# Kernel optimization log

Hardware: AMD Instinct MI355X
Metric: run time of the kernel (lower is better)

Reference implementation:

```python
import jax, jax.numpy as jnp
import numpy as np

N_NODES = 100000
N_EDGES = 1600000
IN_FEATS = 64
HIDDEN = 32
OUT_FEATS = 40


def _linear_init(key, fan_in, fan_out):
    kw, kb = jax.random.split(key)
    bound = 1.0 / np.sqrt(fan_in)
    W = jax.random.uniform(kw, (fan_in, fan_out), jnp.float32, -bound, bound)
    b = jax.random.uniform(kb, (fan_out,), jnp.float32, -bound, bound)
    return W, b


def setup_inputs() -> dict:
    key = jax.random.key(0)
    ks = jax.random.split(key, 8)
    x = jax.random.normal(ks[0], (N_NODES, IN_FEATS), jnp.float32)
    edge_index = jax.random.randint(ks[1], (2, N_EDGES), 0, N_NODES, jnp.int64)
    W_self1, b_self1 = _linear_init(ks[2], IN_FEATS, HIDDEN)
    W_neigh1, b_neigh1 = _linear_init(ks[3], IN_FEATS, HIDDEN)
    W_self2, b_self2 = _linear_init(ks[4], HIDDEN, HIDDEN)
    W_neigh2, b_neigh2 = _linear_init(ks[5], HIDDEN, HIDDEN)
    W_out, b_out = _linear_init(ks[6], HIDDEN, OUT_FEATS)
    W_lin1, b_lin1 = _linear_init(ks[7], IN_FEATS, OUT_FEATS)
    return {"x": x, "edge_index": edge_index,
            "W_self1": W_self1, "b_self1": b_self1,
            "W_neigh1": W_neigh1, "b_neigh1": b_neigh1,
            "W_self2": W_self2, "b_self2": b_self2,
            "W_neigh2": W_neigh2, "b_neigh2": b_neigh2,
            "W_out": W_out, "b_out": b_out,
            "W_lin1": W_lin1, "b_lin1": b_lin1}


def _scatter_mean(feats, src, dst, num_nodes):
    # gather neighbor features [E, F], sum into destinations, divide by degree
    msgs = feats[src]
    agg = jax.ops.segment_sum(msgs, dst, num_segments=num_nodes)
    cnt = jax.ops.segment_sum(jnp.ones((src.shape[0],), feats.dtype), dst,
                              num_segments=num_nodes)
    return agg / jnp.maximum(cnt, 1.0)[:, None]


def _intra_conv(h, src, dst, W_self, b_self, W_neigh, b_neigh, num_nodes):
    # scatter-mean aggregation + fused linear/residual(self)/relu
    x_self = h @ W_self + b_self
    neigh = _scatter_mean(h, src, dst, num_nodes)
    out = neigh @ W_neigh + b_neigh + x_self
    return jax.nn.relu(out)


def reference(x, edge_index, W_self1, b_self1, W_neigh1, b_neigh1,
              W_self2, b_self2, W_neigh2, b_neigh2, W_out, b_out,
              W_lin1, b_lin1):
    num_nodes = x.shape[0]
    src, dst = edge_index[0], edge_index[1]  # PyG source_to_target flow
    initial_x = x @ W_lin1 + b_lin1  # computed in original forward (unused in output)
    h = _intra_conv(x, src, dst, W_self1, b_self1, W_neigh1, b_neigh1, num_nodes)
    h = _intra_conv(h, src, dst, W_self2, b_self2, W_neigh2, b_neigh2, num_nodes)
    # hidden dim == 32 so x32 is the last layer's output (== h); dropout is eval no-op
    x32 = h
    logits = h @ W_out + b_out
    return (x32, logits)
```

## Files before the change

### kernel.cpp

```cpp
#include <hip/hip_runtime.h>

#define NN 100000
#define NE 1600000
#define RB 256
#define NPB 391
#define CAP 8192
#define GS 32

typedef unsigned int uint;
typedef unsigned short ushort;
typedef __fp16 fp16x2 __attribute__((ext_vector_type(2)));

__device__ __forceinline__ float blo(uint u){ return __uint_as_float(u << 16); }
__device__ __forceinline__ float bhi(uint u){ return __uint_as_float(u & 0xffff0000u); }
__device__ __forceinline__ float b2f(ushort u){ return __uint_as_float(((uint)u) << 16); }
__device__ __forceinline__ ushort f2b(float f){
  uint u = __float_as_uint(f);
  uint r = (u + 0x7fffu + ((u >> 16) & 1u)) >> 16;
  return (ushort)r;
}
__device__ __forceinline__ uint packh2(float a, float b){
  union { fp16x2 h; uint u; } c; c.h = __builtin_amdgcn_cvt_pkrtz(a, b); return c.u;
}
__device__ __forceinline__ float h2lo(uint u){
  union { uint u; fp16x2 h; } c; c.u = u; return (float)c.h.x;
}
__device__ __forceinline__ float h2hi(uint u){
  union { uint u; fp16x2 h; } c; c.u = u; return (float)c.h.y;
}
__device__ __forceinline__ float ldf(const void* p, int i, bool isb){
  return isb ? b2f(((const ushort*)p)[i]) : ((const float*)p)[i];
}

__global__ void prep_k(const uint* __restrict__ xw,  const int* __restrict__ ei,
                       const void* __restrict__ Ws1, const void* __restrict__ bs1,
                       const void* __restrict__ Wn1, const void* __restrict__ bn1,
                       const void* __restrict__ Ws2, const void* __restrict__ bs2,
                       const void* __restrict__ Wn2, const void* __restrict__ bn2,
                       const void* __restrict__ Wo,  const void* __restrict__ bo,
                       float* __restrict__ wc1, float* __restrict__ bc1,
                       float* __restrict__ wc2, float* __restrict__ bc2,
                       float* __restrict__ wof, float* __restrict__ bof,
                       float* __restrict__ bn1f, float* __restrict__ bn2f,
                       int* __restrict__ flags, int* __restrict__ gcur)
{
  int t = threadIdx.x;
  __shared__ int nz, bcnt;
  __shared__ int s_isb;
  if (t == 0) { nz = 0; bcnt = 0; }
  __syncthreads();

  int hiw = ei[2 * t + 1];
  if (hiw != 0) atomicOr(&nz, 1);

  uint u = xw[t];
  uint le = (u >> 7) & 0xFFu;
  if (le == 0u || (le >= 96u && le <= 144u)) atomicAdd(&bcnt, 1);
  __syncthreads();
  if (t == 0) s_isb = (bcnt >= 240) ? 1 : 0;
  if (blockIdx.x == 0 && t == 0) {
    flags[0] = (bcnt >= 240) ? 1 : 0;
    flags[1] = (nz == 0) ? 1 : 0;
  }
  __syncthreads();
  bool isb = (s_isb != 0);

  if (blockIdx.x == 0) gcur[t * GS] = t * CAP;

  int g0 = blockIdx.x * 256 + t, gs = gridDim.x * 256;
  for (int i = g0; i < 64 * 64; i += gs) {
    int f = i >> 6, j = i & 63;
    wc1[i] = (j < 32) ? ldf(Ws1, f * 32 + j, isb) : ldf(Wn1, f * 32 + (j - 32), isb);
  }
  for (int i = g0; i < 64; i += gs) bc1[i] = (i < 32) ? ldf(bs1, i, isb) : 0.f;
  for (int i = g0; i < 32 * 64; i += gs) {
    int f = i >> 6, j = i & 63;
    wc2[i] = (j < 32) ? ldf(Ws2, f * 32 + j, isb) : ldf(Wn2, f * 32 + (j - 32), isb);
  }
  for (int i = g0; i < 64; i += gs) bc2[i] = (i < 32) ? ldf(bs2, i, isb) : 0.f;
  for (int i = g0; i < 32 * 40; i += gs) wof[i] = ldf(Wo, i, isb);
  for (int i = g0; i < 40; i += gs) bof[i] = ldf(bo, i, isb);
  for (int i = g0; i < 32; i += gs) bn1f[i] = ldf(bn1, i, isb);
  for (int i = g0; i < 32; i += gs) bn2f[i] = ldf(bn2, i, isb);
}

__device__ __forceinline__ void part_body(const int* __restrict__ ei,
                                          const int* __restrict__ flags,
                                          int2* __restrict__ pairs,
                                          int* __restrict__ gcur, int E, int blk)
{
  __shared__ int hist[RB];
  __shared__ int gbase[RB];
  int m = flags[1];
  int base = blk * 2048;
  hist[threadIdx.x] = 0;
  __syncthreads();
  int bk[8], rk[8]; int2 prs[8];
#pragma unroll
  for (int k = 0; k < 8; k++) {
    int e = base + threadIdx.x + k * 256;
    bk[k] = -1;
    if (e < E) {
      int dd = m ? ei[2 * (E + e)] : ei[E + e];
      int s  = m ? ei[2 * e] : ei[e];
      bk[k] = dd / NPB;
      rk[k] = atomicAdd(&hist[bk[k]], 1);
      prs[k] = make_int2(dd, s);
    }
  }
  __syncthreads();
  if (hist[threadIdx.x] > 0)
    gbase[threadIdx.x] = atomicAdd(&gcur[threadIdx.x * GS], hist[threadIdx.x]);
  __syncthreads();
#pragma unroll
  for (int k = 0; k < 8; k++) {
    if (bk[k] >= 0) {
      int pos = gbase[bk[k]] + rk[k];
      if (pos < (bk[k] + 1) * CAP) pairs[pos] = prs[k];
    }
  }
}

template <int IN, bool XDYN>
__device__ __forceinline__ void transform_body(const void* __restrict__ xin,
                                               const float* __restrict__ W,
                                               const float* __restrict__ bias,
                                               float* __restrict__ tself,
                                               uint* __restrict__ tneigh,
                                               const int* __restrict__ flags, int n)
{
  bool isb = XDYN ? (flags[0] != 0) : false;
  float xr[IN];
  if (XDYN && isb) {
    const uint4* p = (const uint4*)((const ushort*)xin + (size_t)n * IN);
#pragma unroll
    for (int k = 0; k < IN / 8; k++) {
      uint4 v = p[k];
      xr[8 * k + 0] = blo(v.x); xr[8 * k + 1] = bhi(v.x);
      xr[8 * k + 2] = blo(v.y); xr[8 * k + 3] = bhi(v.y);
      xr[8 * k + 4] = blo(v.z); xr[8 * k + 5] = bhi(v.z);
      xr[8 * k + 6] = blo(v.w); xr[8 * k + 7] = bhi(v.w);
    }
  } else {
    const float4* p = (const float4*)((const float*)xin + (size_t)n * IN);
#pragma unroll
    for (int k = 0; k < IN / 4; k++) {
      float4 v = p[k];
      xr[4 * k + 0] = v.x; xr[4 * k + 1] = v.y; xr[4 * k + 2] = v.z; xr[4 * k + 3] = v.w;
    }
  }
#pragma unroll 1
  for (int j0 = 0; j0 < 64; j0 += 32) {
    float acc[32];
#pragma unroll
    for (int jj = 0; jj < 32; jj++) acc[jj] = bias[j0 + jj];
#pragma unroll 8
    for (int f = 0; f < IN; f++) {
      float xv = xr[f];
#pragma unroll
      for (int jj = 0; jj < 32; jj++)
        acc[jj] = fmaf(xv, W[f * 64 + j0 + jj], acc[jj]);
    }
    if (j0 == 0) {
      float* o = tself + (size_t)n * 32;
#pragma unroll
      for (int q = 0; q < 8; q++)
        ((float4*)o)[q] = make_float4(acc[4 * q], acc[4 * q + 1], acc[4 * q + 2], acc[4 * q + 3]);
    } else {
      uint* o = tneigh + (size_t)n * 16;
#pragma unroll
      for (int q = 0; q < 4; q++) {
        uint4 v;
        v.x = packh2(acc[8 * q + 0], acc[8 * q + 1]);
        v.y = packh2(acc[8 * q + 2], acc[8 * q + 3]);
        v.z = packh2(acc[8 * q + 4], acc[8 * q + 5]);
        v.w = packh2(acc[8 * q + 6], acc[8 * q + 7]);
        ((uint4*)o)[q] = v;
      }
    }
  }
}

__global__ __launch_bounds__(256) void part_t1_k(const int* __restrict__ ei,
                                                 const int* __restrict__ flags,
                                                 int2* __restrict__ pairs,
                                                 int* __restrict__ gcur, int E,
                                                 const void* __restrict__ x,
                                                 const float* __restrict__ wc1,
                                                 const float* __restrict__ bc1,
                                                 float* __restrict__ tself,
                                                 uint* __restrict__ tneigh,
                                                 int N, int PB)
{
  if ((int)blockIdx.x < PB) {
    part_body(ei, flags, pairs, gcur, E, (int)blockIdx.x);
  } else {
    int n = ((int)blockIdx.x - PB) * 256 + threadIdx.x;
    if (n < N) transform_body<64, true>(x, wc1, bc1, tself, tneigh, flags, n);
  }
}

__global__ __launch_bounds__(512) void csr_bucket_k(const int2* __restrict__ pairs,
                                                    const int* __restrict__ gcur,
                                                    int2* __restrict__ desc,
                                                    int* __restrict__ col)
{
  __shared__ int lh[NPB];
  __shared__ int ps[512];
  __shared__ int cs[RB];
  int t = threadIdx.x;
  int r = blockIdx.x;
  if (t < RB) cs[t] = min(gcur[t * GS] - t * CAP, CAP);
  __syncthreads();
  if (t < RB) ps[t] = cs[t];
  __syncthreads();
  for (int off = 1; off < RB; off <<= 1) {
    int v = (t < RB && t >= off) ? ps[t - off] : 0;
    __syncthreads();
    if (t < RB) ps[t] += v;
    __syncthreads();
  }
  int n    = cs[r];
  int base = ps[r] - n;
  __syncthreads();

  int lo = r * NPB;
  int nn = min(NPB, NN - lo);
  int b0 = r * CAP;
  for (int j = t; j < NPB; j += 512) lh[j] = 0;
  __syncthreads();
  for (int i = b0 + t; i < b0 + n; i += 512)
    atomicAdd(&lh[pairs[i].x - lo], 1);
  __syncthreads();
  int v = (t < nn) ? lh[t] : 0;
  ps[t] = v;
  __syncthreads();
  for (int off = 1; off < 512; off <<= 1) {
    int x = (t >= off) ? ps[t - off] : 0;
    __syncthreads();
    ps[t] += x;
    __syncthreads();
  }
  int excl = base + ps[t] - v;
  if (t < nn) desc[lo + t] = make_int2(excl, v);
  __syncthreads();
  if (t < nn) lh[t] = excl;
  __syncthreads();
  for (int i = b0 + t; i < b0 + n; i += 512) {
    int2 pr = pairs[i];
    int p = atomicAdd(&lh[pr.x - lo], 1);
    col[p] = pr.y;
  }
}

__device__ __forceinline__ void agg_core2(const float* __restrict__ tself,
                                          const uint* __restrict__ tneigh,
                                          const int2* __restrict__ desc,
                                          const int* __restrict__ col,
                                          const float* __restrict__ bneigh,
                                          int d, int lane,
                                          float& p0, float& p1, float& p2, float& p3,
                                          float& q0, float& q1, float& q2, float& q3)
{
  int slot = lane >> 3, f4 = lane & 7;
  int2 dd0 = desc[d];
  int2 dd1 = desc[d + 1];
  int st0 = dd0.x, dg0 = dd0.y, en0 = st0 + dg0;
  int st1 = dd1.x, dg1 = dd1.y, en1 = st1 + dg1;
  float a0 = 0.f, a1 = 0.f, a2 = 0.f, a3 = 0.f;
  float b0 = 0.f, b1 = 0.f, b2 = 0.f, b3 = 0.f;
  int base0 = st0, base1 = st1;
  while (base0 < en0 || base1 < en1) {
    int cnt0 = max(0, min(64, en0 - base0));
    int cnt1 = max(0, min(64, en1 - base1));
    int ce0 = (lane < cnt0) ? col[base0 + lane] : 0;
    int ce1 = (lane < cnt1) ? col[base1 + lane] : 0;
    int jmax = max(cnt0, cnt1);
#pragma unroll 1
    for (int j = 0; j < jmax; j += 16) {
      int k0 = j + slot, k1 = j + 8 + slot;
      int i00 = __shfl(ce0, k0, 64);
      int i01 = __shfl(ce0, k1, 64);
      int i10 = __shfl(ce1, k0, 64);
      int i11 = __shfl(ce1, k1, 64);
      uint2 u00 = make_uint2(0, 0), u01 = make_uint2(0, 0);
      uint2 u10 = make_uint2(0, 0), u11 = make_uint2(0, 0);
      if (k0 < cnt0) u00 = ((const uint2*)(tneigh + (size_t)i00 * 16))[f4];
      if (k1 < cnt0) u01 = ((const uint2*)(tneigh + (size_t)i01 * 16))[f4];
      if (k0 < cnt1) u10 = ((const uint2*)(tneigh + (size_t)i10 * 16))[f4];
      if (k1 < cnt1) u11 = ((const uint2*)(tneigh + (size_t)i11 * 16))[f4];
      a0 += h2lo(u00.x) + h2lo(u01.x);
      a1 += h2hi(u00.x) + h2hi(u01.x);
      a2 += h2lo(u00.y) + h2lo(u01.y);
      a3 += h2hi(u00.y) + h2hi(u01.y);
      b0 += h2lo(u10.x) + h2lo(u11.x);
      b1 += h2hi(u10.x) + h2hi(u11.x);
      b2 += h2lo(u10.y) + h2lo(u11.y);
      b3 += h2hi(u10.y) + h2hi(u11.y);
    }
    base0 += 64; base1 += 64;
  }
  a0 += __shfl_xor(a0, 8, 64);  a1 += __shfl_xor(a1, 8, 64);
  a2 += __shfl_xor(a2, 8, 64);  a3 += __shfl_xor(a3, 8, 64);
  b0 += __shfl_xor(b0, 8, 64);  b1 += __shfl_xor(b1, 8, 64);
  b2 += __shfl_xor(b2, 8, 64);  b3 += __shfl_xor(b3, 8, 64);
  a0 += __shfl_xor(a0, 16, 64); a1 += __shfl_xor(a1, 16, 64);
  a2 += __shfl_xor(a2, 16, 64); a3 += __shfl_xor(a3, 16, 64);
  b0 += __shfl_xor(b0, 16, 64); b1 += __shfl_xor(b1, 16, 64);
  b2 += __shfl_xor(b2, 16, 64); b3 += __shfl_xor(b3, 16, 64);
  a0 += __shfl_xor(a0, 32, 64); a1 += __shfl_xor(a1, 32, 64);
  a2 += __shfl_xor(a2, 32, 64); a3 += __shfl_xor(a3, 32, 64);
  b0 += __shfl_xor(b0, 32, 64); b1 += __shfl_xor(b1, 32, 64);
  b2 += __shfl_xor(b2, 32, 64); b3 += __shfl_xor(b3, 32, 64);
  float sc0 = 1.0f / (float)max(dg0, 1);
  float sc1 = 1.0f / (float)max(dg1, 1);
  float4 self0 = ((const float4*)(tself + (size_t)d * 32))[f4];
  float4 self1 = ((const float4*)(tself + (size_t)(d + 1) * 32))[f4];
  float4 bn    = ((const float4*)bneigh)[f4];
  p0 = fmaxf(fmaf(a0, sc0, bn.x + self0.x), 0.f);
  p1 = fmaxf(fmaf(a1, sc0, bn.y + self0.y), 0.f);
  p2 = fmaxf(fmaf(a2, sc0, bn.z + self0.z), 0.f);
  p3 = fmaxf(fmaf(a3, sc0, bn.w + self0.w), 0.f);
  q0 = fmaxf(fmaf(b0, sc1, bn.x + self1.x), 0.f);
  q1 = fmaxf(fmaf(b1, sc1, bn.y + self1.y), 0.f);
  q2 = fmaxf(fmaf(b2, sc1, bn.z + self1.z), 0.f);
  q3 = fmaxf(fmaf(b3, sc1, bn.w + self1.w), 0.f);
}

__device__ __forceinline__ float hfeat(int f, float v0, float v1, float v2, float v3)
{
  int src = f >> 2;
  switch (f & 3) {
    case 0:  return __shfl(v0, src, 64);
    case 1:  return __shfl(v1, src, 64);
    case 2:  return __shfl(v2, src, 64);
    default: return __shfl(v3, src, 64);
  }
}

__global__ __launch_bounds__(256) void agg_t2_k(const float* __restrict__ tself1,
                                                const uint* __restrict__ tneigh1,
                                                const int2* __restrict__ desc,
                                                const int* __restrict__ col,
                                                const float* __restrict__ bn1f,
                                                const float* __restrict__ wc2,
                                                const float* __restrict__ bc2,
                                                float* __restrict__ tself2,
                                                uint* __restrict__ tneigh2)
{
  int w = threadIdx.x >> 6;
  int d = blockIdx.x * 8 + w * 2;
  int lane = threadIdx.x & 63;
  float p0, p1, p2, p3, q0, q1, q2, q3;
  agg_core2(tself1, tneigh1, desc, col, bn1f, d, lane,
            p0, p1, p2, p3, q0, q1, q2, q3);
  float accA = bc2[lane];
  float accB = accA;
#pragma unroll
  for (int f = 0; f < 32; f++) {
    float wv = wc2[f * 64 + lane];
    accA = fmaf(hfeat(f, p0, p1, p2, p3), wv, accA);
    accB = fmaf(hfeat(f, q0, q1, q2, q3), wv, accB);
  }
  if (lane < 32) {
    tself2[(size_t)d * 32 + lane] = accA;
    tself2[(size_t)(d + 1) * 32 + lane] = accB;
  }
  float plA = __shfl(accA, 32 + 2 * (lane & 15), 64);
  float phA = __shfl(accA, 33 + 2 * (lane & 15), 64);
  float plB = __shfl(accB, 32 + 2 * (lane & 15), 64);
  float phB = __shfl(accB, 33 + 2 * (lane & 15), 64);
  if (lane < 16) {
    tneigh2[(size_t)d * 16 + lane] = packh2(plA, phA);
    tneigh2[(size_t)(d + 1) * 16 + lane] = packh2(plB, phB);
  }
}

__global__ __launch_bounds__(256) void agg_out_k(const float* __restrict__ tself2,
                                                 const uint* __restrict__ tneigh2,
                                                 const int2* __restrict__ desc,
                                                 const int* __restrict__ col,
                                                 const float* __restrict__ bn2f,
                                                 const float* __restrict__ wof,
                                                 const float* __restrict__ bof,
                                                 void* __restrict__ out,
                                                 const int* __restrict__ flags)
{
  int w = threadIdx.x >> 6;
  int d = blockIdx.x * 8 + w * 2;
  int lane = threadIdx.x & 63;
  float p0, p1, p2, p3, q0, q1, q2, q3;
  agg_core2(tself2, tneigh2, desc, col, bn2f, d, lane,
            p0, p1, p2, p3, q0, q1, q2, q3);
  bool isb = (flags[0] != 0);
  if (lane < 8) {
    if (isb) {
      uint2 pkA, pkB;
      pkA.x = (uint)f2b(p0) | ((uint)f2b(p1) << 16);
      pkA.y = (uint)f2b(p2) | ((uint)f2b(p3) << 16);
      pkB.x = (uint)f2b(q0) | ((uint)f2b(q1) << 16);
      pkB.y = (uint)f2b(q2) | ((uint)f2b(q3) << 16);
      ((uint2*)out)[(size_t)d * 8 + lane] = pkA;
      ((uint2*)out)[(size_t)(d + 1) * 8 + lane] = pkB;
    } else {
      ((float4*)out)[(size_t)d * 8 + lane] = make_float4(p0, p1, p2, p3);
      ((float4*)out)[(size_t)(d + 1) * 8 + lane] = make_float4(q0, q1, q2, q3);
    }
  }
  int lj = (lane < 40) ? lane : 39;
  float accA = bof[lj];
  float accB = accA;
#pragma unroll
  for (int f = 0; f < 32; f++) {
    float wv = wof[f * 40 + lj];
    accA = fmaf(hfeat(f, p0, p1, p2, p3), wv, accA);
    accB = fmaf(hfeat(f, q0, q1, q2, q3), wv, accB);
  }
  if (isb) {
    float loA = __shfl(accA, 2 * lane, 64);
    float hiA = __shfl(accA, 2 * lane + 1, 64);
    float loB = __shfl(accB, 2 * lane, 64);
    float hiB = __shfl(accB, 2 * lane + 1, 64);
    if (lane < 20) {
      ((uint*)out)[(size_t)NN * 16 + (size_t)d * 20 + lane] =
          (uint)f2b(loA) | ((uint)f2b(hiA) << 16);
      ((uint*)out)[(size_t)NN * 16 + (size_t)(d + 1) * 20 + lane] =
          (uint)f2b(loB) | ((uint)f2b(hiB) << 16);
    }
  } else {
    if (lane < 40) {
      ((float*)out)[(size_t)NN * 32 + (size_t)d * 40 + lane] = accA;
      ((float*)out)[(size_t)NN * 32 + (size_t)(d + 1) * 40 + lane] = accB;
    }
  }
}

extern "C" void kernel_launch(void* const* d_in, const int* in_sizes, int n_in,
                              void* d_out, int out_size, void* d_ws, size_t ws_size,
                              hipStream_t stream)
{
  const int N = NN, E = NE;
  const void* x   = d_in[0];
  const int*  ei  = (const int*)d_in[1];

  char* p = (char*)d_ws;
  auto alloc = [&](size_t bytes) -> void* {
    void* r = (void*)p;
    p += (bytes + 255) & ~(size_t)255;
    return r;
  };
  float* wc1  = (float*)alloc(64 * 64 * 4);
  float* bc1  = (float*)alloc(64 * 4);
  float* wc2  = (float*)alloc(32 * 64 * 4);
  float* bc2  = (float*)alloc(64 * 4);
  float* wof  = (float*)alloc(32 * 40 * 4);
  float* bof  = (float*)alloc(40 * 4);
  float* bn1f = (float*)alloc(32 * 4);
  float* bn2f = (float*)alloc(32 * 4);
  int*   flags = (int*)alloc(8);
  int*   gcur = (int*)alloc(RB * GS * 4);
  int2*  desc = (int2*)alloc((size_t)N * 8);
  int*   col  = (int*)alloc((size_t)E * 4);
  int2*  pairs = (int2*)alloc((size_t)RB * CAP * 8);
  float* tself1 = (float*)alloc((size_t)N * 32 * 4);
  uint*  tneigh1 = (uint*)alloc((size_t)N * 16 * 4);
  float* tself2 = (float*)alloc((size_t)N * 32 * 4);
  uint*  tneigh2 = (uint*)pairs;

  const int PB = (E + 2047) / 2048;
  const int TB = (N + 255) / 256;

  prep_k<<<17, 256, 0, stream>>>((const uint*)x, ei,
                                 d_in[2], d_in[3], d_in[4], d_in[5],
                                 d_in[6], d_in[7], d_in[8], d_in[9],
                                 d_in[10], d_in[11],
                                 wc1, bc1, wc2, bc2, wof, bof, bn1f, bn2f,
                                 flags, gcur);
  part_t1_k<<<PB + TB, 256, 0, stream>>>(ei, flags, pairs, gcur, E,
                                         x, wc1, bc1, tself1, tneigh1, N, PB);
  csr_bucket_k<<<RB, 512, 0, stream>>>(pairs, gcur, desc, col);
  agg_t2_k<<<N / 8, 256, 0, stream>>>(tself1, tneigh1, desc, col, bn1f,
                                      wc2, bc2, tself2, tneigh2);
  agg_out_k<<<N / 8, 256, 0, stream>>>(tself2, tneigh2, desc, col, bn2f,
                                       wof, bof, d_out, flags);
}
```

Baseline: 268.0 us.

## Partition edges into fewer large chunks with two-pass bucket histogram

The edge-bucketing partition now uses 128 blocks, each covering a large contiguous edge range, instead of one block per 2048 edges. Each block first builds a shared-memory histogram of destination buckets, reserves global space with one atomic per bucket, then makes a second pass that re-reads the edges and places them using shared-memory atomic cursors. This cuts global atomic contention and gives longer contiguous runs per bucket, which should make the bucket writes more coalesced. In exchange edge indices are read twice, only 128 blocks run the partition, and the order of edges within a bucket is no longer deterministic.

```diff
diff --git a/kernel.cpp b/kernel.cpp
--- a/kernel.cpp
+++ b/kernel.cpp
@@ -6,6 +6,7 @@
 #define NPB 391
 #define CAP 8192
 #define GS 32
+#define NPART 128
 
 typedef unsigned int uint;
 typedef unsigned short ushort;
@@ -90,34 +91,28 @@
                                           int* __restrict__ gcur, int E, int blk)
 {
   __shared__ int hist[RB];
-  __shared__ int gbase[RB];
+  __shared__ int cur[RB];
   int m = flags[1];
-  int base = blk * 2048;
-  hist[threadIdx.x] = 0;
-  __syncthreads();
-  int bk[8], rk[8]; int2 prs[8];
-#pragma unroll
-  for (int k = 0; k < 8; k++) {
-    int e = base + threadIdx.x + k * 256;
-    bk[k] = -1;
-    if (e < E) {
-      int dd = m ? ei[2 * (E + e)] : ei[E + e];
-      int s  = m ? ei[2 * e] : ei[e];
-      bk[k] = dd / NPB;
-      rk[k] = atomicAdd(&hist[bk[k]], 1);
-      prs[k] = make_int2(dd, s);
-    }
-  }
-  __syncthreads();
-  if (hist[threadIdx.x] > 0)
-    gbase[threadIdx.x] = atomicAdd(&gcur[threadIdx.x * GS], hist[threadIdx.x]);
-  __syncthreads();
-#pragma unroll
-  for (int k = 0; k < 8; k++) {
-    if (bk[k] >= 0) {
-      int pos = gbase[bk[k]] + rk[k];
-      if (pos < (bk[k] + 1) * CAP) pairs[pos] = prs[k];
-    }
+  int epb = (E + NPART - 1) / NPART;
+  int e0 = blk * epb;
+  int e1 = min(E, e0 + epb);
+  int t = threadIdx.x;
+  hist[t] = 0;
+  __syncthreads();
+  for (int e = e0 + t; e < e1; e += 256) {
+    int dd = m ? ei[2 * (E + e)] : ei[E + e];
+    atomicAdd(&hist[dd / NPB], 1);
+  }
+  __syncthreads();
+  if (hist[t] > 0)
+    cur[t] = atomicAdd(&gcur[t * GS], hist[t]);
+  __syncthreads();
+  for (int e = e0 + t; e < e1; e += 256) {
+    int dd = m ? ei[2 * (E + e)] : ei[E + e];
+    int s  = m ? ei[2 * e] : ei[e];
+    int bk = dd / NPB;
+    int pos = atomicAdd(&cur[bk], 1);
+    if (pos < (bk + 1) * CAP) pairs[pos] = make_int2(dd, s);
   }
 }
 
@@ -467,7 +462,7 @@
   float* tself2 = (float*)alloc((size_t)N * 32 * 4);
   uint*  tneigh2 = (uint*)pairs;
 
-  const int PB = (E + 2047) / 2048;
+  const int PB = NPART;
   const int TB = (N + 255) / 256;
 
   prep_k<<<17, 256, 0, stream>>>((const uint*)x, ei,
```

Result: slower. 294.5 us (+9.9%).

## Replace global atomic bucket cursors with per-block local sort and offset table

Applied to the files above, without the earlier changes.

The edge partition step no longer reserves space in global bucket cursors with atomics. Each block now sorts its 2048 edges by bucket in shared memory, writes them out contiguously, and records per-bucket offsets. The CSR build kernel then reads each bucket's segments from all 782 blocks through the offset table. This removes contended global atomics and scattered writes, but the CSR kernel now walks many short segments serially per thread, which may load-balance poorly. CSR row starts now use a fixed r*CAP base, so col is padded per bucket.

```diff
diff --git a/kernel.cpp b/kernel.cpp
--- a/kernel.cpp
+++ b/kernel.cpp
@@ -5,7 +5,7 @@
 #define RB 256
 #define NPB 391
 #define CAP 8192
-#define GS 32
+#define NBLK 782
 
 typedef unsigned int uint;
 typedef unsigned short ushort;
@@ -42,7 +42,7 @@
                        float* __restrict__ wc2, float* __restrict__ bc2,
                        float* __restrict__ wof, float* __restrict__ bof,
                        float* __restrict__ bn1f, float* __restrict__ bn2f,
-                       int* __restrict__ flags, int* __restrict__ gcur)
+                       int* __restrict__ flags)
 {
   int t = threadIdx.x;
   __shared__ int nz, bcnt;
@@ -64,8 +64,6 @@
   }
   __syncthreads();
   bool isb = (s_isb != 0);
-
-  if (blockIdx.x == 0) gcur[t * GS] = t * CAP;
 
   int g0 = blockIdx.x * 256 + t, gs = gridDim.x * 256;
   for (int i = g0; i < 64 * 64; i += gs) {
@@ -86,19 +84,22 @@
 
 __device__ __forceinline__ void part_body(const int* __restrict__ ei,
                                           const int* __restrict__ flags,
-                                          int2* __restrict__ pairs,
-                                          int* __restrict__ gcur, int E, int blk)
+                                          int2* __restrict__ pairs2,
+                                          int* __restrict__ off_g, int E, int blk)
 {
   __shared__ int hist[RB];
-  __shared__ int gbase[RB];
+  __shared__ int sc[RB];
+  __shared__ int excl[RB];
+  __shared__ int2 tile[2048];
   int m = flags[1];
   int base = blk * 2048;
-  hist[threadIdx.x] = 0;
+  int t = threadIdx.x;
+  hist[t] = 0;
   __syncthreads();
   int bk[8], rk[8]; int2 prs[8];
 #pragma unroll
   for (int k = 0; k < 8; k++) {
-    int e = base + threadIdx.x + k * 256;
+    int e = base + t + k * 256;
     bk[k] = -1;
     if (e < E) {
       int dd = m ? ei[2 * (E + e)] : ei[E + e];
@@ -109,16 +110,23 @@
     }
   }
   __syncthreads();
-  if (hist[threadIdx.x] > 0)
-    gbase[threadIdx.x] = atomicAdd(&gcur[threadIdx.x * GS], hist[threadIdx.x]);
-  __syncthreads();
-#pragma unroll
-  for (int k = 0; k < 8; k++) {
-    if (bk[k] >= 0) {
-      int pos = gbase[bk[k]] + rk[k];
-      if (pos < (bk[k] + 1) * CAP) pairs[pos] = prs[k];
-    }
-  }
+  sc[t] = hist[t];
+  __syncthreads();
+  for (int o = 1; o < RB; o <<= 1) {
+    int v = (t >= o) ? sc[t - o] : 0;
+    __syncthreads();
+    sc[t] += v;
+    __syncthreads();
+  }
+  excl[t] = sc[t] - hist[t];
+  off_g[blk * RB + t] = excl[t];
+  __syncthreads();
+#pragma unroll
+  for (int k = 0; k < 8; k++)
+    if (bk[k] >= 0) tile[excl[bk[k]] + rk[k]] = prs[k];
+  __syncthreads();
+  int cnt = min(2048, E - base);
+  for (int i = t; i < cnt; i += 256) pairs2[base + i] = tile[i];
 }
 
 template <int IN, bool XDYN>
@@ -183,8 +191,8 @@
 
 __global__ __launch_bounds__(256) void part_t1_k(const int* __restrict__ ei,
                                                  const int* __restrict__ flags,
-                                                 int2* __restrict__ pairs,
-                                                 int* __restrict__ gcur, int E,
+                                                 int2* __restrict__ pairs2,
+                                                 int* __restrict__ off_g, int E,
                                                  const void* __restrict__ x,
                                                  const float* __restrict__ wc1,
                                                  const float* __restrict__ bc1,
@@ -193,44 +201,40 @@
                                                  int N, int PB)
 {
   if ((int)blockIdx.x < PB) {
-    part_body(ei, flags, pairs, gcur, E, (int)blockIdx.x);
+    part_body(ei, flags, pairs2, off_g, E, (int)blockIdx.x);
   } else {
     int n = ((int)blockIdx.x - PB) * 256 + threadIdx.x;
     if (n < N) transform_body<64, true>(x, wc1, bc1, tself, tneigh, flags, n);
   }
 }
 
-__global__ __launch_bounds__(512) void csr_bucket_k(const int2* __restrict__ pairs,
-                                                    const int* __restrict__ gcur,
+__global__ __launch_bounds__(512) void csr_bucket_k(const int2* __restrict__ pairs2,
+                                                    const int* __restrict__ off_g,
                                                     int2* __restrict__ desc,
-                                                    int* __restrict__ col)
-{
-  __shared__ int lh[NPB];
-  __shared__ int ps[512];
-  __shared__ int cs[RB];
+                                                    int* __restrict__ col, int E)
+{
+  __shared__ int   soff[NBLK];
+  __shared__ short slen[NBLK];
+  __shared__ int   lh[NPB];
+  __shared__ int   ps[512];
   int t = threadIdx.x;
   int r = blockIdx.x;
-  if (t < RB) cs[t] = min(gcur[t * GS] - t * CAP, CAP);
-  __syncthreads();
-  if (t < RB) ps[t] = cs[t];
-  __syncthreads();
-  for (int off = 1; off < RB; off <<= 1) {
-    int v = (t < RB && t >= off) ? ps[t - off] : 0;
-    __syncthreads();
-    if (t < RB) ps[t] += v;
-    __syncthreads();
-  }
-  int n    = cs[r];
-  int base = ps[r] - n;
-  __syncthreads();
-
   int lo = r * NPB;
   int nn = min(NPB, NN - lo);
-  int b0 = r * CAP;
+  for (int b = t; b < NBLK; b += 512) {
+    int so = off_g[b * RB + r];
+    int eN = (r == RB - 1) ? min(2048, E - b * 2048) : off_g[b * RB + r + 1];
+    soff[b] = b * 2048 + so;
+    slen[b] = (short)(eN - so);
+  }
   for (int j = t; j < NPB; j += 512) lh[j] = 0;
   __syncthreads();
-  for (int i = b0 + t; i < b0 + n; i += 512)
-    atomicAdd(&lh[pairs[i].x - lo], 1);
+  for (int b = t; b < NBLK; b += 512) {
+    const int2* sp = pairs2 + soff[b];
+    int L = slen[b];
+    for (int i = 0; i < L; i++)
+      atomicAdd(&lh[sp[i].x - lo], 1);
+  }
   __syncthreads();
   int v = (t < nn) ? lh[t] : 0;
   ps[t] = v;
@@ -241,15 +245,19 @@
     ps[t] += x;
     __syncthreads();
   }
-  int excl = base + ps[t] - v;
+  int excl = r * CAP + ps[t] - v;
   if (t < nn) desc[lo + t] = make_int2(excl, v);
   __syncthreads();
   if (t < nn) lh[t] = excl;
   __syncthreads();
-  for (int i = b0 + t; i < b0 + n; i += 512) {
-    int2 pr = pairs[i];
-    int p = atomicAdd(&lh[pr.x - lo], 1);
-    col[p] = pr.y;
+  for (int b = t; b < NBLK; b += 512) {
+    const int2* sp = pairs2 + soff[b];
+    int L = slen[b];
+    for (int i = 0; i < L; i++) {
+      int2 pr = sp[i];
+      int p = atomicAdd(&lh[pr.x - lo], 1);
+      if (p < (r + 1) * CAP) col[p] = pr.y;
+    }
   }
 }
 
@@ -458,16 +466,16 @@
   float* bn1f = (float*)alloc(32 * 4);
   float* bn2f = (float*)alloc(32 * 4);
   int*   flags = (int*)alloc(8);
-  int*   gcur = (int*)alloc(RB * GS * 4);
+  int*   off_g = (int*)alloc((size_t)NBLK * RB * 4);
+  int2*  pairs2 = (int2*)alloc((size_t)NBLK * 2048 * 8);
   int2*  desc = (int2*)alloc((size_t)N * 8);
-  int*   col  = (int*)alloc((size_t)E * 4);
-  int2*  pairs = (int2*)alloc((size_t)RB * CAP * 8);
+  int*   col  = (int*)alloc((size_t)RB * CAP * 4);
   float* tself1 = (float*)alloc((size_t)N * 32 * 4);
   uint*  tneigh1 = (uint*)alloc((size_t)N * 16 * 4);
   float* tself2 = (float*)alloc((size_t)N * 32 * 4);
-  uint*  tneigh2 = (uint*)pairs;
-
-  const int PB = (E + 2047) / 2048;
+  uint*  tneigh2 = (uint*)pairs2;
+
+  const int PB = NBLK;
   const int TB = (N + 255) / 256;
 
   prep_k<<<17, 256, 0, stream>>>((const uint*)x, ei,
@@ -475,10 +483,10 @@
                                  d_in[6], d_in[7], d_in[8], d_in[9],
                                  d_in[10], d_in[11],
                                  wc1, bc1, wc2, bc2, wof, bof, bn1f, bn2f,
-                                 flags, gcur);
-  part_t1_k<<<PB + TB, 256, 0, stream>>>(ei, flags, pairs, gcur, E,
+                                 flags);
+  part_t1_k<<<PB + TB, 256, 0, stream>>>(ei, flags, pairs2, off_g, E,
                                          x, wc1, bc1, tself1, tneigh1, N, PB);
-  csr_bucket_k<<<RB, 512, 0, stream>>>(pairs, gcur, desc, col);
+  csr_bucket_k<<<RB, 512, 0, stream>>>(pairs2, off_g, desc, col, E);
   agg_t2_k<<<N / 8, 256, 0, stream>>>(tself1, tneigh1, desc, col, bn1f,
                                       wc2, bc2, tself2, tneigh2);
   agg_out_k<<<N / 8, 256, 0, stream>>>(tself2, tneigh2, desc, col, bn2f,
```

Result: slower. 285.9 us (+6.7%).
